# Performance work log

Measured on AMD Instinct MI355X. Metric: run time of the kernel, lower is better.

## Reference

```python
import jax, jax.numpy as jnp
import numpy as np

N_NODES = 100000
N_EDGES = 800000
IN_FEATS = 128
HIDDEN = 64
SCALE = 0.5 ** 0.5  # sqrt(0.5) residual scale
BN_EPS = 1e-5


def setup_inputs() -> dict:
    key = jax.random.key(0)
    ks = jax.random.split(key, 12)
    return {
        "src": jax.random.randint(ks[0], (N_EDGES,), 0, N_NODES, dtype=jnp.int64)
        if jax.config.jax_enable_x64 else jax.random.randint(ks[0], (N_EDGES,), 0, N_NODES),
        "dst": jax.random.randint(ks[1], (N_EDGES,), 0, N_NODES),
        "x": jax.random.normal(ks[2], (N_NODES, IN_FEATS), dtype=jnp.float32),
        "fc_w": jax.random.normal(ks[3], (IN_FEATS, HIDDEN), dtype=jnp.float32) * 0.05,
        "fc_b": jax.random.normal(ks[4], (HIDDEN,), dtype=jnp.float32) * 0.05,
        "w1": jax.random.normal(ks[5], (HIDDEN, HIDDEN), dtype=jnp.float32) * 0.05,
        "b1": jax.random.normal(ks[6], (HIDDEN,), dtype=jnp.float32) * 0.05,
        "w2": jax.random.normal(ks[7], (HIDDEN, HIDDEN), dtype=jnp.float32) * 0.05,
        "b2": jax.random.normal(ks[8], (HIDDEN,), dtype=jnp.float32) * 0.05,
        "gamma": jax.random.normal(ks[9], (HIDDEN,), dtype=jnp.float32) * 0.05 + 1.0,
        "beta": jax.random.normal(ks[10], (HIDDEN,), dtype=jnp.float32) * 0.05,
    }


def _graph_conv(h, w, b, src, dst, norm_src, norm_dst, n_nodes):
    # DGL GraphConv, norm='both': y = D_in^{-1/2} A D_out^{-1/2} (h W) + b
    h = h @ w                                   # [N, H]
    m = h[src] * norm_src[:, None]              # gather + src-degree norm, [E, H]
    agg = jax.ops.segment_sum(m, dst, num_segments=n_nodes)  # scatter-add, [N, H]
    return agg * norm_dst[:, None] + b


def reference(src, dst, x, fc_w, fc_b, w1, b1, w2, b2, gamma, beta):
    n_nodes = x.shape[0]
    ones_e = jnp.ones(src.shape[0], dtype=x.dtype)
    deg_out = jnp.clip(jax.ops.segment_sum(ones_e, src, num_segments=n_nodes), 1.0)
    deg_in = jnp.clip(jax.ops.segment_sum(ones_e, dst, num_segments=n_nodes), 1.0)
    norm_src = (deg_out ** -0.5)[src]           # per-edge source normalization
    norm_dst = deg_in ** -0.5                   # per-node destination normalization

    h = x @ fc_w + fc_b                          # fc: [N, H]
    h = (h + _graph_conv(h, w1, b1, src, dst, norm_src, norm_dst, n_nodes)) * SCALE
    h = (h + _graph_conv(h, w2, b2, src, dst, norm_src, norm_dst, n_nodes)) * SCALE

    # BatchNorm1d (training-mode batch statistics over nodes, biased variance)
    mu = h.mean(axis=0)
    var = ((h - mu) ** 2).mean(axis=0)
    h = (h - mu) * jax.lax.rsqrt(var + BN_EPS) * gamma + beta
    return h
```

## Files before the change

### kernel.cpp

```cpp
#include <hip/hip_runtime.h>

#define HIDDEN 64
#define INFEAT 128
#define SCALE_C 0.70710678118654752f
#define BN_EPS 1e-5f
#define AGG_GRID 2048
#define RED_BLK 32

__device__ __forceinline__ float rlf(float v, int l){
  return __int_as_float(__builtin_amdgcn_readlane(__float_as_int(v), l));
}

template<int KDIM, bool ADDB, bool FUSET>
__device__ __forceinline__ void gemm_body(int bid, const float* __restrict__ X,
    const float* __restrict__ W, const float* __restrict__ B,
    float* __restrict__ Y, const float* __restrict__ W2, float* __restrict__ T, int N)
{
  __shared__ float smem[64 * 65];
  const int tid  = threadIdx.x;
  const int lane = tid & 63;
  const int wid  = __builtin_amdgcn_readfirstlane(tid >> 6);
  const int c0 = wid * 16;
  const int base = bid * 64;
  const int gnode = base + lane;

  float acc[16];
  #pragma unroll
  for (int c = 0; c < 16; ++c) acc[c] = ADDB ? B[c0 + c] : 0.f;

  constexpr int NCHUNK = KDIM / 32;
  #pragma unroll 1
  for (int ck = 0; ck < NCHUNK; ++ck){
    __syncthreads();
    #pragma unroll
    for (int i = 0; i < 2; ++i){
      int f  = i * 256 + tid;
      int nd = f >> 3;
      int kq = f & 7;
      float4 v = make_float4(0.f, 0.f, 0.f, 0.f);
      if (base + nd < N)
        v = *(const float4*)(X + (size_t)(base + nd) * KDIM + ck * 32 + kq * 4);
      float* p = &smem[nd * 65 + kq * 4];
      p[0] = v.x; p[1] = v.y; p[2] = v.z; p[3] = v.w;
    }
    __syncthreads();
    const float* wrow = W + (size_t)ck * 32 * HIDDEN + c0;
    #pragma unroll
    for (int k = 0; k < 32; ++k){
      float xv = smem[lane * 65 + k];
      #pragma unroll
      for (int c = 0; c < 16; ++c)
        acc[c] = fmaf(xv, wrow[k * HIDDEN + c], acc[c]);
    }
  }

  if (gnode < N){
    float4* yp = (float4*)(Y + (size_t)gnode * HIDDEN + c0);
    #pragma unroll
    for (int j = 0; j < 4; ++j)
      yp[j] = make_float4(acc[4*j], acc[4*j+1], acc[4*j+2], acc[4*j+3]);
  }

  if constexpr (FUSET){
    __syncthreads();
    #pragma unroll
    for (int c = 0; c < 16; ++c) smem[lane * 65 + c0 + c] = acc[c];
    __syncthreads();
    float tacc[16];
    #pragma unroll
    for (int c = 0; c < 16; ++c) tacc[c] = 0.f;
    const float* w2r = W2 + c0;
    #pragma unroll
    for (int k = 0; k < 64; ++k){
      float hv = smem[lane * 65 + k];
      #pragma unroll
      for (int c = 0; c < 16; ++c)
        tacc[c] = fmaf(hv, w2r[k * HIDDEN + c], tacc[c]);
    }
    if (gnode < N){
      float4* tp = (float4*)(T + (size_t)gnode * HIDDEN + c0);
      #pragma unroll
      for (int j = 0; j < 4; ++j)
        tp[j] = make_float4(tacc[4*j], tacc[4*j+1], tacc[4*j+2], tacc[4*j+3]);
    }
  }
}

__device__ __forceinline__ int role_gemm_idx(int b, int GB, int TOT, int& histIdx){
  int fb  = (int)(((long)b * GB) / TOT);
  int fb1 = (int)(((long)(b + 1) * GB) / TOT);
  histIdx = b - fb;
  return (fb1 > fb) ? fb : -1;
}

__global__ __launch_bounds__(256) void k_mega1(const int* __restrict__ dst,
    int* __restrict__ degI, int* __restrict__ rank, int E,
    const float* __restrict__ x, const float* __restrict__ fc_w,
    const float* __restrict__ fc_b, float* __restrict__ h,
    const float* __restrict__ w1, float* __restrict__ t, int N, int GB, int TOT){
  int hIdx;
  int g = role_gemm_idx(blockIdx.x, GB, TOT, hIdx);
  if (g >= 0) gemm_body<INFEAT, true, true>(g, x, fc_w, fc_b, h, w1, t, N);
  else {
    int e0 = hIdx * 2048 + threadIdx.x;
    #pragma unroll
    for (int i = 0; i < 8; ++i){
      int e = e0 + i * 256;
      if (e < E) rank[e] = atomicAdd(&degI[dst[e]], 1);
    }
  }
}

__global__ __launch_bounds__(256) void k_place(const int* __restrict__ src,
    const int* __restrict__ dst, const int* __restrict__ rank,
    const int* __restrict__ rp, int* __restrict__ cs, int* __restrict__ degO, int E){
  int e0 = blockIdx.x * 2048 + threadIdx.x;
  #pragma unroll
  for (int i = 0; i < 8; ++i){
    int e = e0 + i * 256;
    if (e < E){
      int s = src[e];
      cs[rp[dst[e]] + rank[e]] = s;
      atomicAdd(&degO[s], 1);
    }
  }
}

__global__ void k_scan1(const int* __restrict__ deg, int* __restrict__ bsum, int N){
  __shared__ int sh[256];
  int t = threadIdx.x;
  int i = blockIdx.x * 256 + t;
  sh[t] = (i < N) ? deg[i] : 0;
  __syncthreads();
  for (int ofs = 128; ofs > 0; ofs >>= 1){
    if (t < ofs) sh[t] += sh[t + ofs];
    __syncthreads();
  }
  if (t == 0) bsum[blockIdx.x] = sh[0];
}

__global__ void k_scan2(int* __restrict__ bsum, int NB){
  __shared__ int sh[512];
  int t = threadIdx.x;
  int v = (t < NB) ? bsum[t] : 0;
  sh[t] = v;
  __syncthreads();
  for (int ofs = 1; ofs < 512; ofs <<= 1){
    int u = (t >= ofs) ? sh[t - ofs] : 0;
    __syncthreads();
    sh[t] += u;
    __syncthreads();
  }
  if (t < NB) bsum[t] = sh[t] - v;
}

__global__ void k_scan3(const int* __restrict__ degI, const int* __restrict__ bofs,
                        int* __restrict__ rp, float* __restrict__ norm_in, int N, int E){
  __shared__ int sh[256];
  int t = threadIdx.x;
  int i = blockIdx.x * 256 + t;
  int v = (i < N) ? degI[i] : 0;
  sh[t] = v;
  __syncthreads();
  for (int ofs = 1; ofs < 256; ofs <<= 1){
    int u = (t >= ofs) ? sh[t - ofs] : 0;
    __syncthreads();
    sh[t] += u;
    __syncthreads();
  }
  if (i < N){
    int excl = sh[t] - v + bofs[blockIdx.x];
    rp[i] = excl;
    if (i == N - 1) rp[N] = E;
    norm_in[i] = rsqrtf((float)max(v, 1));
  }
}

template<bool PRE>
__device__ __forceinline__ float4 gather_pre(const int* __restrict__ cs,
    const float* __restrict__ t, const int* __restrict__ degO,
    int start, int end, int g, int s4, int i0, int i1)
{
  float4 acc = make_float4(0.f, 0.f, 0.f, 0.f);
  int j0 = start + g;
  while (j0 < end){
    const bool b1 = (j0 + 4 < end);
    const int k1 = b1 ? i1 : i0;
    const float4 r0 = *(const float4*)(t + (size_t)i0 * HIDDEN + s4);
    const float4 r1 = *(const float4*)(t + (size_t)k1 * HIDDEN + s4);
    const float w0 = PRE ? 1.f : rsqrtf((float)degO[i0]);
    const float w1 = b1 ? (PRE ? 1.f : rsqrtf((float)degO[k1])) : 0.f;
    acc.x = fmaf(r0.x, w0, acc.x); acc.y = fmaf(r0.y, w0, acc.y);
    acc.z = fmaf(r0.z, w0, acc.z); acc.w = fmaf(r0.w, w0, acc.w);
    acc.x = fmaf(r1.x, w1, acc.x); acc.y = fmaf(r1.y, w1, acc.y);
    acc.z = fmaf(r1.z, w1, acc.z); acc.w = fmaf(r1.w, w1, acc.w);
    j0 += 8;
    if (j0 < end){
      i0 = cs[j0];
      i1 = (j0 + 4 < end) ? cs[j0 + 4] : i0;
    }
  }
  return acc;
}

__device__ __forceinline__ float4 xreduce4(float4 a){
  #pragma unroll
  for (int m = 16; m <= 32; m <<= 1){
    a.x += __shfl_xor(a.x, m, 64);
    a.y += __shfl_xor(a.y, m, 64);
    a.z += __shfl_xor(a.z, m, 64);
    a.w += __shfl_xor(a.w, m, 64);
  }
  return a;
}

template<bool BN, bool PRE, bool FUSET2>
__global__ __launch_bounds__(256, 4) void k_agg(const int* __restrict__ rp, const int* __restrict__ cs,
    const float* __restrict__ t, const int* __restrict__ degO,
    const float* __restrict__ norm_in, const float* __restrict__ b,
    const float* __restrict__ w2, float* __restrict__ h,
    float* __restrict__ t2, float* __restrict__ bnpart, int N)
{
  const int tid  = threadIdx.x;
  const int lane = tid & 63;
  const int g    = lane >> 4;
  const int s    = lane & 15;
  const int s4   = s * 4;
  const int wv = (blockIdx.x * 256 + tid) >> 6;
  const int nw = (gridDim.x * 256) >> 6;
  const float4 bv = ((const float4*)b)[s];
  float4 s1 = make_float4(0.f,0.f,0.f,0.f), s2v = make_float4(0.f,0.f,0.f,0.f);

  float w2c[64];
  if constexpr (FUSET2){
    #pragma unroll
    for (int k = 0; k < 64; ++k) w2c[k] = w2[k * HIDDEN + lane];
  }

  int nA = wv;
  int sA = 0, eA = 0, pA0 = 0, pA1 = 0; float niA = 0.f;
  float4 hA = make_float4(0.f,0.f,0.f,0.f);
  if (nA < N){
    sA = rp[nA]; eA = rp[nA + 1];
    niA = norm_in[nA];
    hA = *(const float4*)(h + (size_t)nA * HIDDEN + s4);
    pA0 = (sA + g < eA) ? cs[sA + g] : 0;
    pA1 = (sA + g + 4 < eA) ? cs[sA + g + 4] : 0;
  }
  int nB = nA + nw;
  int sB = 0, eB = 0;
  if (nB < N){ sB = rp[nB]; eB = rp[nB + 1]; }

  for (int n = nA; n < N; n += nw){
    const int nC = n + 2 * nw;
    int sC = 0, eC = 0;
    if (nC < N){ sC = rp[nC]; eC = rp[nC + 1]; }
    int pB0 = 0, pB1 = 0; float niB = 0.f;
    float4 hB = make_float4(0.f,0.f,0.f,0.f);
    if (n + nw < N){
      pB0 = (sB + g < eB) ? cs[sB + g] : 0;
      pB1 = (sB + g + 4 < eB) ? cs[sB + g + 4] : 0;
      niB = norm_in[n + nw];
      hB = *(const float4*)(h + (size_t)(n + nw) * HIDDEN + s4);
    }

    float4 acc = gather_pre<PRE>(cs, t, degO, sA, eA, g, s4, pA0, pA1);
    acc = xreduce4(acc);
    const size_t rowo = (size_t)n * HIDDEN;
    float4 v;
    v.x = (hA.x + acc.x * niA + bv.x) * SCALE_C;
    v.y = (hA.y + acc.y * niA + bv.y) * SCALE_C;
    v.z = (hA.z + acc.z * niA + bv.z) * SCALE_C;
    v.w = (hA.w + acc.w * niA + bv.w) * SCALE_C;
    if (g == 0){
      *(float4*)(h + rowo + s4) = v;
      if (BN){
        s1.x += v.x; s1.y += v.y; s1.z += v.z; s1.w += v.w;
        s2v.x += v.x*v.x; s2v.y += v.y*v.y; s2v.z += v.z*v.z; s2v.w += v.w*v.w;
      }
    }
    if constexpr (FUSET2){
      float nout = rsqrtf((float)max(degO[n], 1));
      float ta0 = 0.f, ta1 = 0.f, ta2 = 0.f, ta3 = 0.f;
      #pragma unroll
      for (int k = 0; k < 64; k += 4){
        const int ln = k >> 2;
        ta0 = fmaf(rlf(v.x, ln), w2c[k],     ta0);
        ta1 = fmaf(rlf(v.y, ln), w2c[k + 1], ta1);
        ta2 = fmaf(rlf(v.z, ln), w2c[k + 2], ta2);
        ta3 = fmaf(rlf(v.w, ln), w2c[k + 3], ta3);
      }
      t2[rowo + lane] = ((ta0 + ta1) + (ta2 + ta3)) * nout;
    }
    sA = sB; eA = eB; pA0 = pB0; pA1 = pB1; niA = niB; hA = hB;
    sB = sC; eB = eC;
  }

  if (BN){
    __shared__ float l1[4][64], l2[4][64];
    const int wid = tid >> 6;
    if (g == 0){
      l1[wid][s4+0] = s1.x; l1[wid][s4+1] = s1.y; l1[wid][s4+2] = s1.z; l1[wid][s4+3] = s1.w;
      l2[wid][s4+0] = s2v.x; l2[wid][s4+1] = s2v.y; l2[wid][s4+2] = s2v.z; l2[wid][s4+3] = s2v.w;
    }
    __syncthreads();
    if (tid < 64){
      float a1 = l1[0][tid] + l1[1][tid] + l1[2][tid] + l1[3][tid];
      float a2 = l2[0][tid] + l2[1][tid] + l2[2][tid] + l2[3][tid];
      bnpart[blockIdx.x * 128 + tid] = a1;
      bnpart[blockIdx.x * 128 + 64 + tid] = a2;
    }
  }
}

__global__ __launch_bounds__(256) void k_bnred(const float* __restrict__ bnpart,
    float* __restrict__ bnred, int nblk){
  int col  = threadIdx.x & 127;
  int half = threadIdx.x >> 7;
  int rows = nblk / RED_BLK;
  int r0 = blockIdx.x * rows;
  float s = 0.f;
  for (int r = half; r < rows; r += 2)
    s += bnpart[(size_t)(r0 + r) * 128 + col];
  __shared__ float sh[256];
  sh[threadIdx.x] = s;
  __syncthreads();
  if (threadIdx.x < 128)
    bnred[blockIdx.x * 128 + threadIdx.x] = sh[threadIdx.x] + sh[threadIdx.x + 128];
}

__global__ void k_bnfin(const float* __restrict__ bnred,
    const float* __restrict__ gamma, const float* __restrict__ beta,
    float* __restrict__ bnab, float invN){
  int c = threadIdx.x;
  float s1 = 0.f, s2 = 0.f;
  #pragma unroll
  for (int b = 0; b < RED_BLK; ++b){ s1 += bnred[b*128 + c]; s2 += bnred[b*128 + 64 + c]; }
  float mu  = s1 * invN;
  float var = s2 * invN - mu * mu;
  float rstd = rsqrtf(var + BN_EPS);
  float sc = gamma[c] * rstd;
  bnab[c] = sc;
  bnab[64 + c] = beta[c] - mu * sc;
}

__global__ void k_bnapply(float* __restrict__ h, const float* __restrict__ bnab, long total4){
  long i = (long)blockIdx.x * blockDim.x + threadIdx.x;
  if (i < total4){
    int c = (int)((i * 4) & 63);
    float4 v = ((float4*)h)[i];
    v.x = fmaf(v.x, bnab[c],     bnab[64 + c]);
    v.y = fmaf(v.y, bnab[c + 1], bnab[65 + c]);
    v.z = fmaf(v.z, bnab[c + 2], bnab[66 + c]);
    v.w = fmaf(v.w, bnab[c + 3], bnab[67 + c]);
    ((float4*)h)[i] = v;
  }
}

extern "C" void kernel_launch(void* const* d_in, const int* in_sizes, int n_in,
                              void* d_out, int out_size, void* d_ws, size_t ws_size,
                              hipStream_t stream){
  const int* src = (const int*)d_in[0];
  const int* dst = (const int*)d_in[1];
  const float* x     = (const float*)d_in[2];
  const float* fc_w  = (const float*)d_in[3];
  const float* fc_b  = (const float*)d_in[4];
  const float* w1    = (const float*)d_in[5];
  const float* b1    = (const float*)d_in[6];
  const float* w2    = (const float*)d_in[7];
  const float* b2    = (const float*)d_in[8];
  const float* gamma = (const float*)d_in[9];
  const float* beta  = (const float*)d_in[10];
  const int E = in_sizes[0];
  const int N = in_sizes[2] / INFEAT;
  const int NB  = (N + 255) / 256;
  const int EB8 = (E + 2047) / 2048;
  const int GB  = (N + 63) / 64;
  const int TOT = EB8 + GB;

  float* h = (float*)d_out;

  const size_t Nh = (size_t)N * HIDDEN;
  float* t        = (float*)d_ws;
  float* t2       = t + Nh;
  float* norm_in  = t2 + Nh;
  float* bnpart   = norm_in + N;
  float* bnred    = bnpart + AGG_GRID * 128;
  float* bnab     = bnred + RED_BLK * 128;
  int*   degO     = (int*)(bnab + 128);
  int*   degI     = degO + N;
  int*   rp       = degI + N;
  int*   bsum     = rp + N + 1;
  int*   rank     = bsum + 512;
  int*   cs       = rank + E;

  hipMemsetAsync(degO, 0, 2 * (size_t)N * sizeof(int), stream);

  k_mega1<<<TOT, 256, 0, stream>>>(dst, degI, rank, E,
                                   x, fc_w, fc_b, h, w1, t, N, GB, TOT);

  k_scan1<<<NB, 256, 0, stream>>>(degI, bsum, N);
  k_scan2<<<1, 512, 0, stream>>>(bsum, NB);
  k_scan3<<<NB, 256, 0, stream>>>(degI, bsum, rp, norm_in, N, E);

  k_place<<<EB8, 256, 0, stream>>>(src, dst, rank, rp, cs, degO, E);

  k_agg<false, false, true><<<AGG_GRID, 256, 0, stream>>>(
      rp, cs, t, degO, norm_in, b1, w2, h, t2, nullptr, N);
  k_agg<true, true, false><<<AGG_GRID, 256, 0, stream>>>(
      rp, cs, t2, degO, norm_in, b2, nullptr, h, nullptr, bnpart, N);

  k_bnred<<<RED_BLK, 256, 0, stream>>>(bnpart, bnred, AGG_GRID);
  k_bnfin<<<1, 64, 0, stream>>>(bnred, gamma, beta, bnab, 1.0f / (float)N);
  long total4 = (long)N * HIDDEN / 4;
  k_bnapply<<<(int)((total4 + 255) / 256), 256, 0, stream>>>(h, bnab, total4);
}
```

Before: 332.4 us.

## Replace rank array with atomic cursor placement and prefetch four neighbor indices

CSR construction now drops the per-edge rank array written in the degree-count pass. Instead k_place claims slots with an atomicAdd on a cursor array that the scan initializes, which removes an E-sized write and read but adds a second atomic per edge. The order of neighbors within each row becomes nondeterministic, so float summation order can vary between runs. The aggregation gather now prefetches four neighbor indices per lane group instead of two, covering the first two iterations without dependent index loads, and the remaining loop loads indices inline.

New measurement: 363.6 us. 1.09x slower.

```diff
diff --git a/kernel.cpp b/kernel.cpp
--- a/kernel.cpp
+++ b/kernel.cpp
@@ -94,7 +94,7 @@
 }
 
 __global__ __launch_bounds__(256) void k_mega1(const int* __restrict__ dst,
-    int* __restrict__ degI, int* __restrict__ rank, int E,
+    int* __restrict__ degI, int E,
     const float* __restrict__ x, const float* __restrict__ fc_w,
     const float* __restrict__ fc_b, float* __restrict__ h,
     const float* __restrict__ w1, float* __restrict__ t, int N, int GB, int TOT){
@@ -106,21 +106,22 @@
     #pragma unroll
     for (int i = 0; i < 8; ++i){
       int e = e0 + i * 256;
-      if (e < E) rank[e] = atomicAdd(&degI[dst[e]], 1);
+      if (e < E) atomicAdd(&degI[dst[e]], 1);
     }
   }
 }
 
 __global__ __launch_bounds__(256) void k_place(const int* __restrict__ src,
-    const int* __restrict__ dst, const int* __restrict__ rank,
-    const int* __restrict__ rp, int* __restrict__ cs, int* __restrict__ degO, int E){
+    const int* __restrict__ dst, int* __restrict__ cursor,
+    int* __restrict__ cs, int* __restrict__ degO, int E){
   int e0 = blockIdx.x * 2048 + threadIdx.x;
   #pragma unroll
   for (int i = 0; i < 8; ++i){
     int e = e0 + i * 256;
     if (e < E){
       int s = src[e];
-      cs[rp[dst[e]] + rank[e]] = s;
+      int pos = atomicAdd(&cursor[dst[e]], 1);
+      cs[pos] = s;
       atomicAdd(&degO[s], 1);
     }
   }
@@ -155,7 +156,8 @@
 }
 
 __global__ void k_scan3(const int* __restrict__ degI, const int* __restrict__ bofs,
-                        int* __restrict__ rp, float* __restrict__ norm_in, int N, int E){
+                        int* __restrict__ rp, int* __restrict__ cursor,
+                        float* __restrict__ norm_in, int N, int E){
   __shared__ int sh[256];
   int t = threadIdx.x;
   int i = blockIdx.x * 256 + t;
@@ -171,36 +173,68 @@
   if (i < N){
     int excl = sh[t] - v + bofs[blockIdx.x];
     rp[i] = excl;
+    cursor[i] = excl;
     if (i == N - 1) rp[N] = E;
     norm_in[i] = rsqrtf((float)max(v, 1));
   }
 }
 
 template<bool PRE>
-__device__ __forceinline__ float4 gather_pre(const int* __restrict__ cs,
+__device__ __forceinline__ float4 gather_pre4(const int* __restrict__ cs,
     const float* __restrict__ t, const int* __restrict__ degO,
-    int start, int end, int g, int s4, int i0, int i1)
+    int start, int end, int g, int s4, int i0, int i1, int i2, int i3)
 {
   float4 acc = make_float4(0.f, 0.f, 0.f, 0.f);
   int j0 = start + g;
-  while (j0 < end){
+  if (j0 >= end) return acc;
+  {
     const bool b1 = (j0 + 4 < end);
-    const int k1 = b1 ? i1 : i0;
     const float4 r0 = *(const float4*)(t + (size_t)i0 * HIDDEN + s4);
-    const float4 r1 = *(const float4*)(t + (size_t)k1 * HIDDEN + s4);
+    const float4 r1 = *(const float4*)(t + (size_t)i1 * HIDDEN + s4);
     const float w0 = PRE ? 1.f : rsqrtf((float)degO[i0]);
-    const float w1 = b1 ? (PRE ? 1.f : rsqrtf((float)degO[k1])) : 0.f;
+    const float w1 = b1 ? (PRE ? 1.f : rsqrtf((float)degO[i1])) : 0.f;
     acc.x = fmaf(r0.x, w0, acc.x); acc.y = fmaf(r0.y, w0, acc.y);
     acc.z = fmaf(r0.z, w0, acc.z); acc.w = fmaf(r0.w, w0, acc.w);
     acc.x = fmaf(r1.x, w1, acc.x); acc.y = fmaf(r1.y, w1, acc.y);
     acc.z = fmaf(r1.z, w1, acc.z); acc.w = fmaf(r1.w, w1, acc.w);
     j0 += 8;
-    if (j0 < end){
-      i0 = cs[j0];
-      i1 = (j0 + 4 < end) ? cs[j0 + 4] : i0;
-    }
+  }
+  if (j0 >= end) return acc;
+  {
+    const bool b1 = (j0 + 4 < end);
+    const float4 r0 = *(const float4*)(t + (size_t)i2 * HIDDEN + s4);
+    const float4 r1 = *(const float4*)(t + (size_t)i3 * HIDDEN + s4);
+    const float w0 = PRE ? 1.f : rsqrtf((float)degO[i2]);
+    const float w1 = b1 ? (PRE ? 1.f : rsqrtf((float)degO[i3])) : 0.f;
+    acc.x = fmaf(r0.x, w0, acc.x); acc.y = fmaf(r0.y, w0, acc.y);
+    acc.z = fmaf(r0.z, w0, acc.z); acc.w = fmaf(r0.w, w0, acc.w);
+    acc.x = fmaf(r1.x, w1, acc.x); acc.y = fmaf(r1.y, w1, acc.y);
+    acc.z = fmaf(r1.z, w1, acc.z); acc.w = fmaf(r1.w, w1, acc.w);
+    j0 += 8;
+  }
+  while (j0 < end){
+    int a0 = cs[j0];
+    int a1 = (j0 + 4 < end) ? cs[j0 + 4] : a0;
+    const bool b1 = (j0 + 4 < end);
+    const float4 r0 = *(const float4*)(t + (size_t)a0 * HIDDEN + s4);
+    const float4 r1 = *(const float4*)(t + (size_t)a1 * HIDDEN + s4);
+    const float w0 = PRE ? 1.f : rsqrtf((float)degO[a0]);
+    const float w1 = b1 ? (PRE ? 1.f : rsqrtf((float)degO[a1])) : 0.f;
+    acc.x = fmaf(r0.x, w0, acc.x); acc.y = fmaf(r0.y, w0, acc.y);
+    acc.z = fmaf(r0.z, w0, acc.z); acc.w = fmaf(r0.w, w0, acc.w);
+    acc.x = fmaf(r1.x, w1, acc.x); acc.y = fmaf(r1.y, w1, acc.y);
+    acc.z = fmaf(r1.z, w1, acc.z); acc.w = fmaf(r1.w, w1, acc.w);
+    j0 += 8;
   }
   return acc;
+}
+
+__device__ __forceinline__ void pf4(const int* __restrict__ cs, int s, int e, int g,
+                                    int& p0, int& p1, int& p2, int& p3){
+  p0 = (s + g      < e) ? cs[s + g]      : 0;
+  p1 = (s + g + 4  < e) ? cs[s + g + 4]  : 0;
+  p2 = (s + g + 8  < e) ? cs[s + g + 8]  : 0;
+  p3 = (s + g + 12 < e) ? cs[s + g + 12] : 0;
 }
 
 __device__ __forceinline__ float4 xreduce4(float4 a){
@@ -238,14 +272,13 @@
   }
 
   int nA = wv;
-  int sA = 0, eA = 0, pA0 = 0, pA1 = 0; float niA = 0.f;
+  int sA = 0, eA = 0, pA0 = 0, pA1 = 0, pA2 = 0, pA3 = 0; float niA = 0.f;
   float4 hA = make_float4(0.f,0.f,0.f,0.f);
   if (nA < N){
     sA = rp[nA]; eA = rp[nA + 1];
     niA = norm_in[nA];
     hA = *(const float4*)(h + (size_t)nA * HIDDEN + s4);
-    pA0 = (sA + g < eA) ? cs[sA + g] : 0;
-    pA1 = (sA + g + 4 < eA) ? cs[sA + g + 4] : 0;
+    pf4(cs, sA, eA, g, pA0, pA1, pA2, pA3);
   }
   int nB = nA + nw;
   int sB = 0, eB = 0;
@@ -255,16 +288,15 @@
     const int nC = n + 2 * nw;
     int sC = 0, eC = 0;
     if (nC < N){ sC = rp[nC]; eC = rp[nC + 1]; }
-    int pB0 = 0, pB1 = 0; float niB = 0.f;
+    int pB0 = 0, pB1 = 0, pB2 = 0, pB3 = 0; float niB = 0.f;
     float4 hB = make_float4(0.f,0.f,0.f,0.f);
     if (n + nw < N){
-      pB0 = (sB + g < eB) ? cs[sB + g] : 0;
-      pB1 = (sB + g + 4 < eB) ? cs[sB + g + 4] : 0;
+      pf4(cs, sB, eB, g, pB0, pB1, pB2, pB3);
       niB = norm_in[n + nw];
       hB = *(const float4*)(h + (size_t)(n + nw) * HIDDEN + s4);
     }
 
-    float4 acc = gather_pre<PRE>(cs, t, degO, sA, eA, g, s4, pA0, pA1);
+    float4 acc = gather_pre4<PRE>(cs, t, degO, sA, eA, g, s4, pA0, pA1, pA2, pA3);
     acc = xreduce4(acc);
     const size_t rowo = (size_t)n * HIDDEN;
     float4 v;
@@ -292,7 +324,7 @@
       }
       t2[rowo + lane] = ((ta0 + ta1) + (ta2 + ta3)) * nout;
     }
-    sA = sB; eA = eB; pA0 = pB0; pA1 = pB1; niA = niB; hA = hB;
+    sA = sB; eA = eB; pA0 = pB0; pA1 = pB1; pA2 = pB2; pA3 = pB3; niA = niB; hA = hB;
     sB = sC; eB = eC;
   }
 
@@ -390,20 +422,20 @@
   int*   degO     = (int*)(bnab + 128);
   int*   degI     = degO + N;
   int*   rp       = degI + N;
-  int*   bsum     = rp + N + 1;
-  int*   rank     = bsum + 512;
-  int*   cs       = rank + E;
+  int*   cursor   = rp + N + 1;
+  int*   bsum     = cursor + N;
+  int*   cs       = bsum + 512;
 
   hipMemsetAsync(degO, 0, 2 * (size_t)N * sizeof(int), stream);
 
-  k_mega1<<<TOT, 256, 0, stream>>>(dst, degI, rank, E,
+  k_mega1<<<TOT, 256, 0, stream>>>(dst, degI, E,
                                    x, fc_w, fc_b, h, w1, t, N, GB, TOT);
 
   k_scan1<<<NB, 256, 0, stream>>>(degI, bsum, N);
   k_scan2<<<1, 512, 0, stream>>>(bsum, NB);
-  k_scan3<<<NB, 256, 0, stream>>>(degI, bsum, rp, norm_in, N, E);
-
-  k_place<<<EB8, 256, 0, stream>>>(src, dst, rank, rp, cs, degO, E);
+  k_scan3<<<NB, 256, 0, stream>>>(degI, bsum, rp, cursor, norm_in, N, E);
+
+  k_place<<<EB8, 256, 0, stream>>>(src, dst, cursor, cs, degO, E);
 
   k_agg<false, false, true><<<AGG_GRID, 256, 0, stream>>>(
       rp, cs, t, degO, norm_in, b1, w2, h, t2, nullptr, N);
```
